# Kernel optimization log

Hardware: AMD Instinct MI355X
Metric: run time of the kernel (lower is better)

Reference implementation:

```python
import jax, jax.numpy as jnp
import numpy as np

N = 50000
IN_DIM = 256
HID = 64
HEADS = 4
OUT_DIM = 64
NEG_SLOPE = 0.2


def gat_conv(x, src, dst, W, att_src, att_dst, bias, heads, out_ch):
    # x: [N, F_in]; src/dst: [E] (self-loops already appended)
    n = x.shape[0]
    h = (x @ W).reshape(n, heads, out_ch)                     # [N,H,C]
    a_s = jnp.sum(h * att_src, axis=-1)                       # [N,H]
    a_d = jnp.sum(h * att_dst, axis=-1)                       # [N,H]
    e = jax.nn.leaky_relu(a_s[src] + a_d[dst], NEG_SLOPE)     # [E,H]
    # segment softmax over destination neighborhoods
    m = jax.ops.segment_max(e, dst, num_segments=n)           # [N,H]
    m = jnp.where(jnp.isfinite(m), m, 0.0)
    ex = jnp.exp(e - m[dst])                                  # [E,H]
    denom = jax.ops.segment_sum(ex, dst, num_segments=n)      # [N,H]
    alpha = ex / (denom[dst] + 1e-16)                         # [E,H]
    msg = alpha[:, :, None] * h[src]                          # [E,H,C]
    out = jax.ops.segment_sum(msg, dst, num_segments=n)       # [N,H,C]
    return out.reshape(n, heads * out_ch) + bias


def setup_inputs() -> dict:
    key = jax.random.key(0)
    ks = jax.random.split(key, 10)
    glorot = lambda k, shape: jax.random.normal(k, shape, jnp.float32) * np.sqrt(2.0 / (shape[0] + shape[-1]))
    x = jax.random.normal(ks[0], (N, IN_DIM), jnp.float32)
    edge_index = jax.random.randint(ks[1], (2, 800000), 0, N, jnp.int64)
    W1 = glorot(ks[2], (IN_DIM, HEADS * HID))
    att_src1 = glorot(ks[3], (HEADS, HID))
    att_dst1 = glorot(ks[4], (HEADS, HID))
    b1 = jnp.zeros((HEADS * HID,), jnp.float32)
    W2 = glorot(ks[5], (HEADS * HID, OUT_DIM))
    att_src2 = glorot(ks[6], (1, OUT_DIM))
    att_dst2 = glorot(ks[7], (1, OUT_DIM))
    b2 = jnp.zeros((OUT_DIM,), jnp.float32)
    return {"x": x, "edge_index": edge_index, "W1": W1, "att_src1": att_src1,
            "att_dst1": att_dst1, "b1": b1, "W2": W2, "att_src2": att_src2,
            "att_dst2": att_dst2, "b2": b2}


def reference(x, edge_index, W1, att_src1, att_dst1, b1, W2, att_src2, att_dst2, b2):
    # add self loops (PyG GATConv default)
    loops = jnp.arange(N, dtype=edge_index.dtype)
    src = jnp.concatenate([edge_index[0], loops])
    dst = jnp.concatenate([edge_index[1], loops])
    h = gat_conv(x, src, dst, W1, att_src1, att_dst1, b1, HEADS, HID)
    h = jax.nn.elu(h)
    out = gat_conv(h, src, dst, W2, att_src2, att_dst2, b2, 1, OUT_DIM)
    return out
```

## Files before the change

kernel.cpp:

```cpp
#include <hip/hip_runtime.h>
#include <math.h>

#define N_NODES 50000
#define E_RAW   800000
#define E_TOT   850000
#define NEG_SLOPE 0.2f
#define NBC 196

typedef __attribute__((ext_vector_type(8))) short short8;
typedef __attribute__((ext_vector_type(4))) float f32x4;

__device__ __forceinline__ float lrelu(float v) {
    return v >= 0.f ? v : NEG_SLOPE * v;
}
__device__ __forceinline__ unsigned short f2bf(float f) {
    union { float f; unsigned u; } v; v.f = f;
    unsigned r = v.u + 0x7FFF + ((v.u >> 16) & 1);
    return (unsigned short)(r >> 16);
}
__device__ __forceinline__ float bf2f(unsigned short h) {
    union { unsigned u; float f; } v; v.u = ((unsigned)h) << 16;
    return v.f;
}
__device__ __forceinline__ int C1(int p) { return (p & 15) * 16 + (p >> 4); }
__device__ __forceinline__ int C2(int p) { return (p & 3) * 16 + (p >> 2); }

__global__ __launch_bounds__(256) void k_prep_hist(
    const int* __restrict__ dst, int* __restrict__ counts,
    const float* __restrict__ W1, const float* __restrict__ W2,
    unsigned short* __restrict__ Wf1, unsigned short* __restrict__ Wf2)
{
    int idx = blockIdx.x * 256 + threadIdx.x;
    if (idx < 8192) {
        int lane = idx & 63, kb = (idx >> 6) & 7, nb = idx >> 9;
        int c = nb * 16 + (lane & 15);
        int k0 = kb * 32 + ((lane >> 4) & 3) * 8;
        short8 pk;
#pragma unroll
        for (int j = 0; j < 8; ++j)
            pk[j] = (short)f2bf(W1[(k0 + j) * 256 + c]);
        *(short8*)&Wf1[idx * 8] = pk;
    } else if (idx < 10240) {
        int i2 = idx - 8192;
        int lane = i2 & 63, kb = (i2 >> 6) & 7, nb = i2 >> 9;
        int c = nb * 16 + (lane & 15);
        int k0 = kb * 32 + ((lane >> 4) & 3) * 8;
        short8 pk;
#pragma unroll
        for (int j = 0; j < 8; ++j)
            pk[j] = (short)f2bf(W2[C1(k0 + j) * 64 + c]);
        *(short8*)&Wf2[i2 * 8] = pk;
    }
    if (idx < E_TOT) {
        int d = (idx < E_RAW) ? dst[idx] : idx - E_RAW;
        atomicAdd(&counts[d], 1);
    }
}

__global__ __launch_bounds__(256) void k_scan1(
    const int* __restrict__ counts, int* __restrict__ off, int* __restrict__ bsum)
{
    __shared__ int sh[256];
    int t = threadIdx.x, i = blockIdx.x * 256 + t;
    int c = (i < N_NODES) ? counts[i] : 0;
    sh[t] = c; __syncthreads();
    for (int ofs = 1; ofs < 256; ofs <<= 1) {
        int v = (t >= ofs) ? sh[t - ofs] : 0;
        __syncthreads(); sh[t] += v; __syncthreads();
    }
    if (i < N_NODES) off[i] = sh[t] - c;
    if (t == 255) bsum[blockIdx.x] = sh[255];
}

__global__ __launch_bounds__(256) void k_scan2(int* __restrict__ bsum)
{
    __shared__ int sh[256];
    int t = threadIdx.x;
    int c = (t < NBC) ? bsum[t] : 0;
    sh[t] = c; __syncthreads();
    for (int ofs = 1; ofs < 256; ofs <<= 1) {
        int v = (t >= ofs) ? sh[t - ofs] : 0;
        __syncthreads(); sh[t] += v; __syncthreads();
    }
    if (t < NBC) bsum[t] = sh[t] - c;
}

__global__ __launch_bounds__(256) void k_scan3(
    int* __restrict__ off, const int* __restrict__ bsum)
{
    int i = blockIdx.x * 256 + threadIdx.x;
    if (i < N_NODES) off[i] += bsum[blockIdx.x];
    if (i == 0) off[N_NODES] = E_TOT;
}

__global__ __launch_bounds__(256) void k_scatter(
    const int* __restrict__ src, const int* __restrict__ dst,
    const int* __restrict__ off, int* __restrict__ cursor,
    const float* __restrict__ as1, const float* __restrict__ ad1,
    unsigned short* __restrict__ esrc, float* __restrict__ aw1)
{
    int e = blockIdx.x * 256 + threadIdx.x;
    if (e >= E_TOT) return;
    int s, d;
    if (e < E_RAW) { s = src[e]; d = dst[e]; } else { s = e - E_RAW; d = s; }
    int pos = off[d] + atomicAdd(&cursor[d], 1);
    esrc[pos] = (unsigned short)s;
    float4 A = *(const float4*)&as1[s * 4];
    float4 B = *(const float4*)&ad1[d * 4];
    float4 w;
    w.x = __expf(lrelu(A.x + B.x));
    w.y = __expf(lrelu(A.y + B.y));
    w.z = __expf(lrelu(A.z + B.z));
    w.w = __expf(lrelu(A.w + B.w));
    *(float4*)&aw1[pos * 4] = w;
}

__global__ __launch_bounds__(256) void k_gemm1(
    const float* __restrict__ x, const unsigned short* __restrict__ Wf1,
    const float* __restrict__ att_src, const float* __restrict__ att_dst,
    unsigned short* __restrict__ h1b, float* __restrict__ as1, float* __restrict__ ad1)
{
    const int t = threadIdx.x;
    const int lane = t & 63;
    const int w = t >> 6;
    const int rbase = blockIdx.x * 16;
    const int q  = lane & 15;
    const int kg = lane >> 4;
    const int rowA = rbase + q;

    f32x4 acc[4];
#pragma unroll
    for (int nb = 0; nb < 4; ++nb) acc[nb] = (f32x4){0.f, 0.f, 0.f, 0.f};

    short8 b[2][4];
    float4 a0, a1, a0n, a1n;
    {
        const float* ap = &x[rowA * 256 + kg * 8];
        a0 = *(const float4*)ap;
        a1 = *(const float4*)(ap + 4);
#pragma unroll
        for (int nb = 0; nb < 4; ++nb)
            b[0][nb] = *(const short8*)&Wf1[(((w * 4 + nb) * 8 + 0) * 64 + lane) * 8];
    }
#pragma unroll
    for (int kb = 0; kb < 8; ++kb) {
        if (kb < 7) {
            const float* ap = &x[rowA * 256 + (kb + 1) * 32 + kg * 8];
            a0n = *(const float4*)ap;
            a1n = *(const float4*)(ap + 4);
#pragma unroll
            for (int nb = 0; nb < 4; ++nb)
                b[(kb + 1) & 1][nb] =
                    *(const short8*)&Wf1[(((w * 4 + nb) * 8 + kb + 1) * 64 + lane) * 8];
        }
        short8 af;
        af[0] = (short)f2bf(a0.x); af[1] = (short)f2bf(a0.y);
        af[2] = (short)f2bf(a0.z); af[3] = (short)f2bf(a0.w);
        af[4] = (short)f2bf(a1.x); af[5] = (short)f2bf(a1.y);
        af[6] = (short)f2bf(a1.z); af[7] = (short)f2bf(a1.w);
#pragma unroll
        for (int nb = 0; nb < 4; ++nb)
            acc[nb] = __builtin_amdgcn_mfma_f32_16x16x32_bf16(af, b[kb & 1][nb], acc[nb], 0, 0, 0);
        if (kb < 7) { a0 = a0n; a1 = a1n; }
    }

#pragma unroll
    for (int reg = 0; reg < 4; ++reg) {
        int n = rbase + kg * 4 + reg;
        ushort4 pk;
        pk.x = f2bf(acc[0][reg]); pk.y = f2bf(acc[1][reg]);
        pk.z = f2bf(acc[2][reg]); pk.w = f2bf(acc[3][reg]);
        *(ushort4*)&h1b[n * 256 + q * 16 + w * 4] = pk;
    }
    float asv[4], adv[4];
#pragma unroll
    for (int nb = 0; nb < 4; ++nb) {
        int col = (w * 4 + nb) * 16 + q;
        asv[nb] = att_src[col];
        adv[nb] = att_dst[col];
    }
#pragma unroll
    for (int reg = 0; reg < 4; ++reg) {
        float s = acc[0][reg]*asv[0] + acc[1][reg]*asv[1] + acc[2][reg]*asv[2] + acc[3][reg]*asv[3];
        float d = acc[0][reg]*adv[0] + acc[1][reg]*adv[1] + acc[2][reg]*adv[2] + acc[3][reg]*adv[3];
#pragma unroll
        for (int ofs = 1; ofs < 16; ofs <<= 1) {
            s += __shfl_xor(s, ofs);
            d += __shfl_xor(d, ofs);
        }
        if (q == 0) {
            int n = rbase + kg * 4 + reg;
            as1[n * 4 + w] = s;
            ad1[n * 4 + w] = d;
        }
    }
}

__global__ __launch_bounds__(256) void k_gather1(
    const unsigned short* __restrict__ esrc, const int* __restrict__ off,
    const float* __restrict__ aw1,
    const unsigned short* __restrict__ h1b, const float* __restrict__ b1,
    unsigned short* __restrict__ hmid)
{
    int d    = (blockIdx.x * 256 + threadIdx.x) >> 6;
    int lane = threadIdx.x & 63;
    const int head = lane & 3;
    const int e0 = off[d], e1 = off[d + 1];
    float4 acc = make_float4(0.f, 0.f, 0.f, 0.f);
    float dn = 0.f;
    int e = e0;
    for (; e + 3 < e1; e += 4) {
        int s0 = esrc[e], s1 = esrc[e + 1], s2 = esrc[e + 2], s3 = esrc[e + 3];
        float w0 = aw1[(e + 0) * 4 + head];
        float w1 = aw1[(e + 1) * 4 + head];
        float w2 = aw1[(e + 2) * 4 + head];
        float w3 = aw1[(e + 3) * 4 + head];
        ushort4 u0 = *(const ushort4*)&h1b[s0 * 256 + lane * 4];
        ushort4 u1 = *(const ushort4*)&h1b[s1 * 256 + lane * 4];
        ushort4 u2 = *(const ushort4*)&h1b[s2 * 256 + lane * 4];
        ushort4 u3 = *(const ushort4*)&h1b[s3 * 256 + lane * 4];
        dn += (w0 + w1) + (w2 + w3);
        acc.x = fmaf(w0, bf2f(u0.x), fmaf(w1, bf2f(u1.x), fmaf(w2, bf2f(u2.x), fmaf(w3, bf2f(u3.x), acc.x))));
        acc.y = fmaf(w0, bf2f(u0.y), fmaf(w1, bf2f(u1.y), fmaf(w2, bf2f(u2.y), fmaf(w3, bf2f(u3.y), acc.y))));
        acc.z = fmaf(w0, bf2f(u0.z), fmaf(w1, bf2f(u1.z), fmaf(w2, bf2f(u2.z), fmaf(w3, bf2f(u3.z), acc.z))));
        acc.w = fmaf(w0, bf2f(u0.w), fmaf(w1, bf2f(u1.w), fmaf(w2, bf2f(u2.w), fmaf(w3, bf2f(u3.w), acc.w))));
    }
    for (; e < e1; ++e) {
        int s0 = esrc[e];
        float w0 = aw1[e * 4 + head];
        ushort4 u0 = *(const ushort4*)&h1b[s0 * 256 + lane * 4];
        dn += w0;
        acc.x = fmaf(w0, bf2f(u0.x), acc.x);
        acc.y = fmaf(w0, bf2f(u0.y), acc.y);
        acc.z = fmaf(w0, bf2f(u0.z), acc.z);
        acc.w = fmaf(w0, bf2f(u0.w), acc.w);
    }
    const float inv = 1.f / (dn + 1e-16f);
    float o[4] = {acc.x, acc.y, acc.z, acc.w};
    ushort4 pk;
    unsigned short* pko = (unsigned short*)&pk;
#pragma unroll
    for (int i = 0; i < 4; ++i) {
        float v = o[i] * inv + b1[C1(lane * 4 + i)];
        v = v > 0.f ? v : expm1f(v);
        pko[i] = f2bf(v);
    }
    *(ushort4*)&hmid[d * 256 + lane * 4] = pk;
}

__global__ __launch_bounds__(256) void k_gemm2(
    const unsigned short* __restrict__ hmid, const unsigned short* __restrict__ Wf2,
    const float* __restrict__ att_src, const float* __restrict__ att_dst,
    unsigned short* __restrict__ h2b, float* __restrict__ as2, float* __restrict__ ad2)
{
    const int t = threadIdx.x;
    const int lane = t & 63;
    const int w = t >> 6;
    const int rbase = blockIdx.x * 64 + w * 16;
    const int q  = lane & 15;
    const int kg = lane >> 4;
    const int rowA = rbase + q;
    const int rA = rowA < N_NODES ? rowA : N_NODES - 1;

    f32x4 acc[4];
#pragma unroll
    for (int nb = 0; nb < 4; ++nb) acc[nb] = (f32x4){0.f, 0.f, 0.f, 0.f};

    short8 b[2][4];
    short8 af, afn;
    af = *(const short8*)&hmid[rA * 256 + kg * 8];
#pragma unroll
    for (int nb = 0; nb < 4; ++nb)
        b[0][nb] = *(const short8*)&Wf2[((nb * 8 + 0) * 64 + lane) * 8];
#pragma unroll
    for (int kb = 0; kb < 8; ++kb) {
        if (kb < 7) {
            afn = *(const short8*)&hmid[rA * 256 + (kb + 1) * 32 + kg * 8];
#pragma unroll
            for (int nb = 0; nb < 4; ++nb)
                b[(kb + 1) & 1][nb] = *(const short8*)&Wf2[((nb * 8 + kb + 1) * 64 + lane) * 8];
        }
#pragma unroll
        for (int nb = 0; nb < 4; ++nb)
            acc[nb] = __builtin_amdgcn_mfma_f32_16x16x32_bf16(af, b[kb & 1][nb], acc[nb], 0, 0, 0);
        if (kb < 7) af = afn;
    }

    float asv[4], adv[4];
#pragma unroll
    for (int nb = 0; nb < 4; ++nb) {
        int col = nb * 16 + q;
        asv[nb] = att_src[col];
        adv[nb] = att_dst[col];
    }
#pragma unroll
    for (int reg = 0; reg < 4; ++reg) {
        int n = rbase + kg * 4 + reg;
        bool ok = n < N_NODES;
        if (ok) {
            ushort4 pk;
            pk.x = f2bf(acc[0][reg]); pk.y = f2bf(acc[1][reg]);
            pk.z = f2bf(acc[2][reg]); pk.w = f2bf(acc[3][reg]);
            *(ushort4*)&h2b[n * 64 + q * 4] = pk;
        }
        float s = acc[0][reg]*asv[0] + acc[1][reg]*asv[1] + acc[2][reg]*asv[2] + acc[3][reg]*asv[3];
        float d = acc[0][reg]*adv[0] + acc[1][reg]*adv[1] + acc[2][reg]*adv[2] + acc[3][reg]*adv[3];
#pragma unroll
        for (int ofs = 1; ofs < 16; ofs <<= 1) {
            s += __shfl_xor(s, ofs);
            d += __shfl_xor(d, ofs);
        }
        if (ok && q == 0) { as2[n] = s; ad2[n] = d; }
    }
}

__global__ __launch_bounds__(256) void k_gather2(
    const unsigned short* __restrict__ esrc, const int* __restrict__ off,
    const float* __restrict__ as2, const float* __restrict__ ad2,
    const unsigned short* __restrict__ h2b, const float* __restrict__ b2,
    float* __restrict__ out)
{
    const int t = threadIdx.x;
    const int w = t >> 6;
    const int lane = t & 63;
    const int g  = lane >> 4;
    const int j2 = lane & 15;
    const int d = blockIdx.x * 16 + w * 4 + g;
    const float adv = ad2[d];
    const int e0 = off[d], e1 = off[d + 1];
    const unsigned short* hb = h2b + j2 * 4;

    float acc[4] = {0.f, 0.f, 0.f, 0.f};
    float dn = 0.f;
    int e = e0;
    for (; e + 3 < e1; e += 4) {
        int s0 = esrc[e], s1 = esrc[e + 1], s2 = esrc[e + 2], s3 = esrc[e + 3];
        float w0 = __expf(lrelu(as2[s0] + adv));
        float w1 = __expf(lrelu(as2[s1] + adv));
        float w2 = __expf(lrelu(as2[s2] + adv));
        float w3 = __expf(lrelu(as2[s3] + adv));
        ushort4 u0 = *(const ushort4*)(hb + s0 * 64);
        ushort4 u1 = *(const ushort4*)(hb + s1 * 64);
        ushort4 u2 = *(const ushort4*)(hb + s2 * 64);
        ushort4 u3 = *(const ushort4*)(hb + s3 * 64);
        dn += (w0 + w1) + (w2 + w3);
        acc[0] = fmaf(w0, bf2f(u0.x), fmaf(w1, bf2f(u1.x), fmaf(w2, bf2f(u2.x), fmaf(w3, bf2f(u3.x), acc[0]))));
        acc[1] = fmaf(w0, bf2f(u0.y), fmaf(w1, bf2f(u1.y), fmaf(w2, bf2f(u2.y), fmaf(w3, bf2f(u3.y), acc[1]))));
        acc[2] = fmaf(w0, bf2f(u0.z), fmaf(w1, bf2f(u1.z), fmaf(w2, bf2f(u2.z), fmaf(w3, bf2f(u3.z), acc[2]))));
        acc[3] = fmaf(w0, bf2f(u0.w), fmaf(w1, bf2f(u1.w), fmaf(w2, bf2f(u2.w), fmaf(w3, bf2f(u3.w), acc[3]))));
    }
    for (; e < e1; ++e) {
        int s0 = esrc[e];
        float w0 = __expf(lrelu(as2[s0] + adv));
        ushort4 u0 = *(const ushort4*)(hb + s0 * 64);
        dn += w0;
        acc[0] = fmaf(w0, bf2f(u0.x), acc[0]);
        acc[1] = fmaf(w0, bf2f(u0.y), acc[1]);
        acc[2] = fmaf(w0, bf2f(u0.z), acc[2]);
        acc[3] = fmaf(w0, bf2f(u0.w), acc[3]);
    }
    const float inv = 1.f / (dn + 1e-16f);
#pragma unroll
    for (int i = 0; i < 4; ++i) {
        int col = i * 16 + j2;
        out[d * 64 + col] = acc[i] * inv + b2[col];
    }
}

extern "C" void kernel_launch(void* const* d_in, const int* in_sizes, int n_in,
                              void* d_out, int out_size, void* d_ws, size_t ws_size,
                              hipStream_t stream)
{
    const float* x        = (const float*)d_in[0];
    const int*   ei       = (const int*)d_in[1];
    const float* W1       = (const float*)d_in[2];
    const float* att_src1 = (const float*)d_in[3];
    const float* att_dst1 = (const float*)d_in[4];
    const float* b1       = (const float*)d_in[5];
    const float* W2       = (const float*)d_in[6];
    const float* att_src2 = (const float*)d_in[7];
    const float* att_dst2 = (const float*)d_in[8];
    const float* b2       = (const float*)d_in[9];
    const int* src = ei;
    const int* dst = ei + E_RAW;
    float* out = (float*)d_out;

    char* ws = (char*)d_ws;
    int*            counts = (int*)(ws + 0);
    int*            cursor = (int*)(ws + 200000);
    int*            off    = (int*)(ws + 400000);
    int*            bsum   = (int*)(ws + 600064);
    float*          as1    = (float*)(ws + 600896);
    float*          ad1    = (float*)(ws + 1400896);
    float*          as2    = (float*)(ws + 2200896);
    float*          ad2    = (float*)(ws + 2400896);
    unsigned short* esrc   = (unsigned short*)(ws + 2600896);
    unsigned short* Wf1    = (unsigned short*)(ws + 4300896);
    unsigned short* Wf2    = (unsigned short*)(ws + 4431968);
    float*          aw1    = (float*)(ws + 4464736);
    unsigned short* h1b    = (unsigned short*)(ws + 18064736);
    unsigned short* h2b    = (unsigned short*)(ws + 18064736);
    unsigned short* hmid   = (unsigned short*)(ws + 43664736);

    hipMemsetAsync(ws, 0, 400000, stream);

    const int EB = (E_TOT + 255) / 256;
    k_prep_hist<<<EB, 256, 0, stream>>>(dst, counts, W1, W2, Wf1, Wf2);
    k_scan1  <<<NBC, 256, 0, stream>>>(counts, off, bsum);
    k_scan2  <<<1, 256, 0, stream>>>(bsum);
    k_scan3  <<<NBC, 256, 0, stream>>>(off, bsum);
    k_gemm1  <<<3125, 256, 0, stream>>>(x, Wf1, att_src1, att_dst1, h1b, as1, ad1);
    k_scatter<<<EB, 256, 0, stream>>>(src, dst, off, cursor, as1, ad1, esrc, aw1);
    k_gather1<<<12500, 256, 0, stream>>>(esrc, off, aw1, h1b, b1, hmid);
    k_gemm2  <<<782, 256, 0, stream>>>(hmid, Wf2, att_src2, att_dst2, h2b, as2, ad2);
    k_gather2<<<3125, 256, 0, stream>>>(esrc, off, as2, ad2, h2b, b2, out);
}
```

Baseline: 249.1 us.

## Precompute layer-2 edge weights in separate kernel and unroll gather1 by eight

Adds a k_alpha2 kernel that computes exp(leaky_relu(as2[src]+ad2[dst])) once per edge into a new aw2 buffer. k_gather2 then reads these weights directly instead of having 16 lanes each redundantly gather as2 and evaluate exp. Gather1 gets an 8-way unrolled main loop so more independent row loads are in flight at once. The off pointer is shifted by 32 bytes, presumably for alignment. The trade is an extra kernel launch and an extra round trip of per-edge weights through memory, plus higher register pressure in gather1.

```diff
diff --git a/kernel.cpp b/kernel.cpp
--- a/kernel.cpp
+++ b/kernel.cpp
@@ -209,12 +209,35 @@
     float4 acc = make_float4(0.f, 0.f, 0.f, 0.f);
     float dn = 0.f;
     int e = e0;
+    for (; e + 7 < e1; e += 8) {
+        int s0 = esrc[e],     s1 = esrc[e + 1], s2 = esrc[e + 2], s3 = esrc[e + 3];
+        int s4 = esrc[e + 4], s5 = esrc[e + 5], s6 = esrc[e + 6], s7 = esrc[e + 7];
+        float w0 = aw1[(e + 0) * 4 + head], w1 = aw1[(e + 1) * 4 + head];
+        float w2 = aw1[(e + 2) * 4 + head], w3 = aw1[(e + 3) * 4 + head];
+        float w4 = aw1[(e + 4) * 4 + head], w5 = aw1[(e + 5) * 4 + head];
+        float w6 = aw1[(e + 6) * 4 + head], w7 = aw1[(e + 7) * 4 + head];
+        ushort4 u0 = *(const ushort4*)&h1b[s0 * 256 + lane * 4];
+        ushort4 u1 = *(const ushort4*)&h1b[s1 * 256 + lane * 4];
+        ushort4 u2 = *(const ushort4*)&h1b[s2 * 256 + lane * 4];
+        ushort4 u3 = *(const ushort4*)&h1b[s3 * 256 + lane * 4];
+        ushort4 u4 = *(const ushort4*)&h1b[s4 * 256 + lane * 4];
+        ushort4 u5 = *(const ushort4*)&h1b[s5 * 256 + lane * 4];
+        ushort4 u6 = *(const ushort4*)&h1b[s6 * 256 + lane * 4];
+        ushort4 u7 = *(const ushort4*)&h1b[s7 * 256 + lane * 4];
+        dn += ((w0 + w1) + (w2 + w3)) + ((w4 + w5) + (w6 + w7));
+        acc.x = fmaf(w0, bf2f(u0.x), fmaf(w1, bf2f(u1.x), fmaf(w2, bf2f(u2.x), fmaf(w3, bf2f(u3.x), acc.x))));
+        acc.y = fmaf(w0, bf2f(u0.y), fmaf(w1, bf2f(u1.y), fmaf(w2, bf2f(u2.y), fmaf(w3, bf2f(u3.y), acc.y))));
+        acc.z = fmaf(w0, bf2f(u0.z), fmaf(w1, bf2f(u1.z), fmaf(w2, bf2f(u2.z), fmaf(w3, bf2f(u3.z), acc.z))));
+        acc.w = fmaf(w0, bf2f(u0.w), fmaf(w1, bf2f(u1.w), fmaf(w2, bf2f(u2.w), fmaf(w3, bf2f(u3.w), acc.w))));
+        acc.x = fmaf(w4, bf2f(u4.x), fmaf(w5, bf2f(u5.x), fmaf(w6, bf2f(u6.x), fmaf(w7, bf2f(u7.x), acc.x))));
+        acc.y = fmaf(w4, bf2f(u4.y), fmaf(w5, bf2f(u5.y), fmaf(w6, bf2f(u6.y), fmaf(w7, bf2f(u7.y), acc.y))));
+        acc.z = fmaf(w4, bf2f(u4.z), fmaf(w5, bf2f(u5.z), fmaf(w6, bf2f(u6.z), fmaf(w7, bf2f(u7.z), acc.z))));
+        acc.w = fmaf(w4, bf2f(u4.w), fmaf(w5, bf2f(u5.w), fmaf(w6, bf2f(u6.w), fmaf(w7, bf2f(u7.w), acc.w))));
+    }
     for (; e + 3 < e1; e += 4) {
         int s0 = esrc[e], s1 = esrc[e + 1], s2 = esrc[e + 2], s3 = esrc[e + 3];
-        float w0 = aw1[(e + 0) * 4 + head];
-        float w1 = aw1[(e + 1) * 4 + head];
-        float w2 = aw1[(e + 2) * 4 + head];
-        float w3 = aw1[(e + 3) * 4 + head];
+        float w0 = aw1[(e + 0) * 4 + head], w1 = aw1[(e + 1) * 4 + head];
+        float w2 = aw1[(e + 2) * 4 + head], w3 = aw1[(e + 3) * 4 + head];
         ushort4 u0 = *(const ushort4*)&h1b[s0 * 256 + lane * 4];
         ushort4 u1 = *(const ushort4*)&h1b[s1 * 256 + lane * 4];
         ushort4 u2 = *(const ushort4*)&h1b[s2 * 256 + lane * 4];
@@ -314,9 +337,24 @@
     }
 }
 
+__global__ __launch_bounds__(256) void k_alpha2(
+    const unsigned short* __restrict__ esrc, const int* __restrict__ off,
+    const float* __restrict__ as2, const float* __restrict__ ad2,
+    float* __restrict__ aw2)
+{
+    int d    = (blockIdx.x * 256 + threadIdx.x) >> 6;
+    int lane = threadIdx.x & 63;
+    const float adv = ad2[d];
+    const int e0 = off[d], e1 = off[d + 1];
+    for (int e = e0 + lane; e < e1; e += 64) {
+        int s = esrc[e];
+        aw2[e] = __expf(lrelu(as2[s] + adv));
+    }
+}
+
 __global__ __launch_bounds__(256) void k_gather2(
     const unsigned short* __restrict__ esrc, const int* __restrict__ off,
-    const float* __restrict__ as2, const float* __restrict__ ad2,
+    const float* __restrict__ aw2,
     const unsigned short* __restrict__ h2b, const float* __restrict__ b2,
     float* __restrict__ out)
 {
@@ -326,7 +364,6 @@
     const int g  = lane >> 4;
     const int j2 = lane & 15;
     const int d = blockIdx.x * 16 + w * 4 + g;
-    const float adv = ad2[d];
     const int e0 = off[d], e1 = off[d + 1];
     const unsigned short* hb = h2b + j2 * 4;
 
@@ -335,10 +372,7 @@
     int e = e0;
     for (; e + 3 < e1; e += 4) {
         int s0 = esrc[e], s1 = esrc[e + 1], s2 = esrc[e + 2], s3 = esrc[e + 3];
-        float w0 = __expf(lrelu(as2[s0] + adv));
-        float w1 = __expf(lrelu(as2[s1] + adv));
-        float w2 = __expf(lrelu(as2[s2] + adv));
-        float w3 = __expf(lrelu(as2[s3] + adv));
+        float w0 = aw2[e], w1 = aw2[e + 1], w2 = aw2[e + 2], w3 = aw2[e + 3];
         ushort4 u0 = *(const ushort4*)(hb + s0 * 64);
         ushort4 u1 = *(const ushort4*)(hb + s1 * 64);
         ushort4 u2 = *(const ushort4*)(hb + s2 * 64);
@@ -351,7 +385,7 @@
     }
     for (; e < e1; ++e) {
         int s0 = esrc[e];
-        float w0 = __expf(lrelu(as2[s0] + adv));
+        float w0 = aw2[e];
         ushort4 u0 = *(const ushort4*)(hb + s0 * 64);
         dn += w0;
         acc[0] = fmaf(w0, bf2f(u0.x), acc[0]);
@@ -388,7 +422,7 @@
     char* ws = (char*)d_ws;
     int*            counts = (int*)(ws + 0);
     int*            cursor = (int*)(ws + 200000);
-    int*            off    = (int*)(ws + 400000);
+    int*            off    = (int*)(ws + 400032);
     int*            bsum   = (int*)(ws + 600064);
     float*          as1    = (float*)(ws + 600896);
     float*          ad1    = (float*)(ws + 1400896);
@@ -401,6 +435,7 @@
     unsigned short* h1b    = (unsigned short*)(ws + 18064736);
     unsigned short* h2b    = (unsigned short*)(ws + 18064736);
     unsigned short* hmid   = (unsigned short*)(ws + 43664736);
+    float*          aw2    = (float*)(ws + 69264736);
 
     hipMemsetAsync(ws, 0, 400000, stream);
 
@@ -413,5 +448,6 @@
     k_scatter<<<EB, 256, 0, stream>>>(src, dst, off, cursor, as1, ad1, esrc, aw1);
     k_gather1<<<12500, 256, 0, stream>>>(esrc, off, aw1, h1b, b1, hmid);
     k_gemm2  <<<782, 256, 0, stream>>>(hmid, Wf2, att_src2, att_dst2, h2b, as2, ad2);
-    k_gather2<<<3125, 256, 0, stream>>>(esrc, off, as2, ad2, h2b, b2, out);
-}
+    k_alpha2 <<<12500, 256, 0, stream>>>(esrc, off, as2, ad2, aw2);
+    k_gather2<<<3125, 256, 0, stream>>>(esrc, off, aw2, h2b, b2, out);
+}
```

After: 258.5 us. 1.04x slower.

## Fuse layer-1 aggregation with layer-2 GEMM through shared memory

Applied to the files above, without the earlier changes.

Merges the layer-1 neighbor gather and the layer-2 projection GEMM into one kernel. Each block aggregates 16 destination nodes into a shared-memory tile, then runs an MFMA per wave against Wf2 and computes the attention scores with a cross-wave reduction in shared memory. This removes the hmid intermediate round-trip through global memory and one kernel launch. In exchange each wave handles 4 nodes serially, so fewer wavefronts are in flight to hide gather latency, and the h2b stores become scattered 2-byte writes. The off buffer offset also moves.

```diff
diff --git a/kernel.cpp b/kernel.cpp
--- a/kernel.cpp
+++ b/kernel.cpp
@@ -196,121 +196,96 @@
     }
 }
 
-__global__ __launch_bounds__(256) void k_gather1(
+__global__ __launch_bounds__(256) void k_gat1g2(
     const unsigned short* __restrict__ esrc, const int* __restrict__ off,
     const float* __restrict__ aw1,
     const unsigned short* __restrict__ h1b, const float* __restrict__ b1,
-    unsigned short* __restrict__ hmid)
-{
-    int d    = (blockIdx.x * 256 + threadIdx.x) >> 6;
-    int lane = threadIdx.x & 63;
+    const unsigned short* __restrict__ Wf2,
+    const float* __restrict__ att_src2, const float* __restrict__ att_dst2,
+    unsigned short* __restrict__ h2b, float* __restrict__ as2, float* __restrict__ ad2)
+{
+    __shared__ unsigned short hs[16][264];
+    __shared__ float ss[16][4], sd[16][4];
+    const int t = threadIdx.x;
+    const int w = t >> 6;
+    const int lane = t & 63;
+    const int d0 = blockIdx.x * 16;
     const int head = lane & 3;
-    const int e0 = off[d], e1 = off[d + 1];
-    float4 acc = make_float4(0.f, 0.f, 0.f, 0.f);
-    float dn = 0.f;
-    int e = e0;
-    for (; e + 3 < e1; e += 4) {
-        int s0 = esrc[e], s1 = esrc[e + 1], s2 = esrc[e + 2], s3 = esrc[e + 3];
-        float w0 = aw1[(e + 0) * 4 + head];
-        float w1 = aw1[(e + 1) * 4 + head];
-        float w2 = aw1[(e + 2) * 4 + head];
-        float w3 = aw1[(e + 3) * 4 + head];
-        ushort4 u0 = *(const ushort4*)&h1b[s0 * 256 + lane * 4];
-        ushort4 u1 = *(const ushort4*)&h1b[s1 * 256 + lane * 4];
-        ushort4 u2 = *(const ushort4*)&h1b[s2 * 256 + lane * 4];
-        ushort4 u3 = *(const ushort4*)&h1b[s3 * 256 + lane * 4];
-        dn += (w0 + w1) + (w2 + w3);
-        acc.x = fmaf(w0, bf2f(u0.x), fmaf(w1, bf2f(u1.x), fmaf(w2, bf2f(u2.x), fmaf(w3, bf2f(u3.x), acc.x))));
-        acc.y = fmaf(w0, bf2f(u0.y), fmaf(w1, bf2f(u1.y), fmaf(w2, bf2f(u2.y), fmaf(w3, bf2f(u3.y), acc.y))));
-        acc.z = fmaf(w0, bf2f(u0.z), fmaf(w1, bf2f(u1.z), fmaf(w2, bf2f(u2.z), fmaf(w3, bf2f(u3.z), acc.z))));
-        acc.w = fmaf(w0, bf2f(u0.w), fmaf(w1, bf2f(u1.w), fmaf(w2, bf2f(u2.w), fmaf(w3, bf2f(u3.w), acc.w))));
-    }
-    for (; e < e1; ++e) {
-        int s0 = esrc[e];
-        float w0 = aw1[e * 4 + head];
-        ushort4 u0 = *(const ushort4*)&h1b[s0 * 256 + lane * 4];
-        dn += w0;
-        acc.x = fmaf(w0, bf2f(u0.x), acc.x);
-        acc.y = fmaf(w0, bf2f(u0.y), acc.y);
-        acc.z = fmaf(w0, bf2f(u0.z), acc.z);
-        acc.w = fmaf(w0, bf2f(u0.w), acc.w);
-    }
-    const float inv = 1.f / (dn + 1e-16f);
-    float o[4] = {acc.x, acc.y, acc.z, acc.w};
-    ushort4 pk;
-    unsigned short* pko = (unsigned short*)&pk;
-#pragma unroll
-    for (int i = 0; i < 4; ++i) {
-        float v = o[i] * inv + b1[C1(lane * 4 + i)];
-        v = v > 0.f ? v : expm1f(v);
-        pko[i] = f2bf(v);
-    }
-    *(ushort4*)&hmid[d * 256 + lane * 4] = pk;
-}
-
-__global__ __launch_bounds__(256) void k_gemm2(
-    const unsigned short* __restrict__ hmid, const unsigned short* __restrict__ Wf2,
-    const float* __restrict__ att_src, const float* __restrict__ att_dst,
-    unsigned short* __restrict__ h2b, float* __restrict__ as2, float* __restrict__ ad2)
-{
-    const int t = threadIdx.x;
-    const int lane = t & 63;
-    const int w = t >> 6;
-    const int rbase = blockIdx.x * 64 + w * 16;
+
+    for (int r = 0; r < 4; ++r) {
+        const int ld = w * 4 + r;
+        const int d = d0 + ld;
+        const int e0 = off[d], e1 = off[d + 1];
+        float4 acc = make_float4(0.f, 0.f, 0.f, 0.f);
+        float dn = 0.f;
+        int e = e0;
+        for (; e + 3 < e1; e += 4) {
+            int s0 = esrc[e], s1 = esrc[e + 1], s2 = esrc[e + 2], s3 = esrc[e + 3];
+            float w0 = aw1[(e + 0) * 4 + head], w1 = aw1[(e + 1) * 4 + head];
+            float w2 = aw1[(e + 2) * 4 + head], w3 = aw1[(e + 3) * 4 + head];
+            ushort4 u0 = *(const ushort4*)&h1b[s0 * 256 + lane * 4];
+            ushort4 u1 = *(const ushort4*)&h1b[s1 * 256 + lane * 4];
+            ushort4 u2 = *(const ushort4*)&h1b[s2 * 256 + lane * 4];
+            ushort4 u3 = *(const ushort4*)&h1b[s3 * 256 + lane * 4];
+            dn += (w0 + w1) + (w2 + w3);
+            acc.x = fmaf(w0, bf2f(u0.x), fmaf(w1, bf2f(u1.x), fmaf(w2, bf2f(u2.x), fmaf(w3, bf2f(u3.x), acc.x))));
+            acc.y = fmaf(w0, bf2f(u0.y), fmaf(w1, bf2f(u1.y), fmaf(w2, bf2f(u2.y), fmaf(w3, bf2f(u3.y), acc.y))));
+            acc.z = fmaf(w0, bf2f(u0.z), fmaf(w1, bf2f(u1.z), fmaf(w2, bf2f(u2.z), fmaf(w3, bf2f(u3.z), acc.z))));
+            acc.w = fmaf(w0, bf2f(u0.w), fmaf(w1, bf2f(u1.w), fmaf(w2, bf2f(u2.w), fmaf(w3, bf2f(u3.w), acc.w))));
+        }
+        for (; e < e1; ++e) {
+            int s0 = esrc[e];
+            float w0 = aw1[e * 4 + head];
+            ushort4 u0 = *(const ushort4*)&h1b[s0 * 256 + lane * 4];
+            dn += w0;
+            acc.x = fmaf(w0, bf2f(u0.x), acc.x);
+            acc.y = fmaf(w0, bf2f(u0.y), acc.y);
+            acc.z = fmaf(w0, bf2f(u0.z), acc.z);
+            acc.w = fmaf(w0, bf2f(u0.w), acc.w);
+        }
+        const float inv = 1.f / (dn + 1e-16f);
+        float o[4] = {acc.x, acc.y, acc.z, acc.w};
+        ushort4 pk;
+        unsigned short* pko = (unsigned short*)&pk;
+#pragma unroll
+        for (int i = 0; i < 4; ++i) {
+            float v = o[i] * inv + b1[C1(lane * 4 + i)];
+            v = v > 0.f ? v : expm1f(v);
+            pko[i] = f2bf(v);
+        }
+        *(ushort4*)&hs[ld][lane * 4] = pk;
+    }
+    __syncthreads();
+
     const int q  = lane & 15;
     const int kg = lane >> 4;
-    const int rowA = rbase + q;
-    const int rA = rowA < N_NODES ? rowA : N_NODES - 1;
-
-    f32x4 acc[4];
-#pragma unroll
-    for (int nb = 0; nb < 4; ++nb) acc[nb] = (f32x4){0.f, 0.f, 0.f, 0.f};
-
-    short8 b[2][4];
-    short8 af, afn;
-    af = *(const short8*)&hmid[rA * 256 + kg * 8];
-#pragma unroll
-    for (int nb = 0; nb < 4; ++nb)
-        b[0][nb] = *(const short8*)&Wf2[((nb * 8 + 0) * 64 + lane) * 8];
+    f32x4 acc2 = (f32x4){0.f, 0.f, 0.f, 0.f};
 #pragma unroll
     for (int kb = 0; kb < 8; ++kb) {
-        if (kb < 7) {
-            afn = *(const short8*)&hmid[rA * 256 + (kb + 1) * 32 + kg * 8];
-#pragma unroll
-            for (int nb = 0; nb < 4; ++nb)
-                b[(kb + 1) & 1][nb] = *(const short8*)&Wf2[((nb * 8 + kb + 1) * 64 + lane) * 8];
-        }
-#pragma unroll
-        for (int nb = 0; nb < 4; ++nb)
-            acc[nb] = __builtin_amdgcn_mfma_f32_16x16x32_bf16(af, b[kb & 1][nb], acc[nb], 0, 0, 0);
-        if (kb < 7) af = afn;
-    }
-
-    float asv[4], adv[4];
-#pragma unroll
-    for (int nb = 0; nb < 4; ++nb) {
-        int col = nb * 16 + q;
-        asv[nb] = att_src[col];
-        adv[nb] = att_dst[col];
-    }
+        short8 af = *(const short8*)&hs[q][kb * 32 + kg * 8];
+        short8 bf = *(const short8*)&Wf2[((w * 8 + kb) * 64 + lane) * 8];
+        acc2 = __builtin_amdgcn_mfma_f32_16x16x32_bf16(af, bf, acc2, 0, 0, 0);
+    }
+    const float asv = att_src2[w * 16 + q];
+    const float adv = att_dst2[w * 16 + q];
 #pragma unroll
     for (int reg = 0; reg < 4; ++reg) {
-        int n = rbase + kg * 4 + reg;
-        bool ok = n < N_NODES;
-        if (ok) {
-            ushort4 pk;
-            pk.x = f2bf(acc[0][reg]); pk.y = f2bf(acc[1][reg]);
-            pk.z = f2bf(acc[2][reg]); pk.w = f2bf(acc[3][reg]);
-            *(ushort4*)&h2b[n * 64 + q * 4] = pk;
-        }
-        float s = acc[0][reg]*asv[0] + acc[1][reg]*asv[1] + acc[2][reg]*asv[2] + acc[3][reg]*asv[3];
-        float d = acc[0][reg]*adv[0] + acc[1][reg]*adv[1] + acc[2][reg]*adv[2] + acc[3][reg]*adv[3];
+        int row = kg * 4 + reg;
+        int n = d0 + row;
+        h2b[n * 64 + q * 4 + w] = f2bf(acc2[reg]);
+        float s = acc2[reg] * asv;
+        float d = acc2[reg] * adv;
 #pragma unroll
         for (int ofs = 1; ofs < 16; ofs <<= 1) {
             s += __shfl_xor(s, ofs);
             d += __shfl_xor(d, ofs);
         }
-        if (ok && q == 0) { as2[n] = s; ad2[n] = d; }
+        if (q == 0) { ss[row][w] = s; sd[row][w] = d; }
+    }
+    __syncthreads();
+    if (t < 16) {
+        as2[d0 + t] = (ss[t][0] + ss[t][1]) + (ss[t][2] + ss[t][3]);
+        ad2[d0 + t] = (sd[t][0] + sd[t][1]) + (sd[t][2] + sd[t][3]);
     }
 }
 
@@ -388,7 +363,7 @@
     char* ws = (char*)d_ws;
     int*            counts = (int*)(ws + 0);
     int*            cursor = (int*)(ws + 200000);
-    int*            off    = (int*)(ws + 400000);
+    int*            off    = (int*)(ws + 400032);
     int*            bsum   = (int*)(ws + 600064);
     float*          as1    = (float*)(ws + 600896);
     float*          ad1    = (float*)(ws + 1400896);
@@ -399,8 +374,7 @@
     unsigned short* Wf2    = (unsigned short*)(ws + 4431968);
     float*          aw1    = (float*)(ws + 4464736);
     unsigned short* h1b    = (unsigned short*)(ws + 18064736);
-    unsigned short* h2b    = (unsigned short*)(ws + 18064736);
-    unsigned short* hmid   = (unsigned short*)(ws + 43664736);
+    unsigned short* h2b    = (unsigned short*)(ws + 43664736);
 
     hipMemsetAsync(ws, 0, 400000, stream);
 
@@ -411,7 +385,7 @@
     k_scan3  <<<NBC, 256, 0, stream>>>(off, bsum);
     k_gemm1  <<<3125, 256, 0, stream>>>(x, Wf1, att_src1, att_dst1, h1b, as1, ad1);
     k_scatter<<<EB, 256, 0, stream>>>(src, dst, off, cursor, as1, ad1, esrc, aw1);
-    k_gather1<<<12500, 256, 0, stream>>>(esrc, off, aw1, h1b, b1, hmid);
-    k_gemm2  <<<782, 256, 0, stream>>>(hmid, Wf2, att_src2, att_dst2, h2b, as2, ad2);
+    k_gat1g2 <<<3125, 256, 0, stream>>>(esrc, off, aw1, h1b, b1, Wf2,
+                                        att_src2, att_dst2, h2b, as2, ad2);
     k_gather2<<<3125, 256, 0, stream>>>(esrc, off, as2, ad2, h2b, b2, out);
 }
```

Result: faster. 243.8 us (-2.1%).
